# Performance work log

Hardware: AMD Instinct MI355X
Metric: run time of the kernel (lower is better)

## Reference

```python
import jax, jax.numpy as jnp
import numpy as np

HID, QK_NOPE, QK_ROPE, Q_LR, KV_LR, H, V_DIM = 2048, 128, 64, 768, 512, 16, 128
QK_HEAD = QK_NOPE + QK_ROPE
THETA = 10000.0
EPS = 1e-5


def _layernorm(x, g, b):
    mu = jnp.mean(x, axis=-1, keepdims=True)
    var = jnp.mean(jnp.square(x - mu), axis=-1, keepdims=True)
    return (x - mu) * jax.lax.rsqrt(var + EPS) * g + b


def _rotate_half(x):
    x1, x2 = jnp.split(x, 2, axis=-1)
    return jnp.concatenate([-x2, x1], axis=-1)


def setup_inputs() -> dict:
    key = jax.random.key(0)
    ks = jax.random.split(key, 6)
    s = 0.02
    return {
        "hidden_state": jax.random.normal(ks[0], (2, 4096, HID), dtype=jnp.float32),
        "w_qa": jax.random.normal(ks[1], (Q_LR, HID), dtype=jnp.float32) * s,
        "b_qa": jnp.zeros((Q_LR,), jnp.float32),
        "g_qa_ln": jnp.ones((Q_LR,), jnp.float32),
        "b_qa_ln": jnp.zeros((Q_LR,), jnp.float32),
        "w_qb": jax.random.normal(ks[2], (H * QK_HEAD, Q_LR), dtype=jnp.float32) * s,
        "b_qb": jnp.zeros((H * QK_HEAD,), jnp.float32),
        "w_kva": jax.random.normal(ks[3], (KV_LR + QK_ROPE, HID), dtype=jnp.float32) * s,
        "b_kva": jnp.zeros((KV_LR + QK_ROPE,), jnp.float32),
        "g_kva_ln": jnp.ones((KV_LR,), jnp.float32),
        "b_kva_ln": jnp.zeros((KV_LR,), jnp.float32),
        "w_kvb": jax.random.normal(ks[4], (H * (QK_NOPE + V_DIM), KV_LR), dtype=jnp.float32) * s,
        "b_kvb": jnp.zeros((H * (QK_NOPE + V_DIM),), jnp.float32),
    }


def reference(hidden_state, w_qa, b_qa, g_qa_ln, b_qa_ln, w_qb, b_qb,
              w_kva, b_kva, g_kva_ln, b_kva_ln, w_kvb, b_kvb):
    B, S, _ = hidden_state.shape
    # ----- Q path: low-rank down-proj -> LN -> up-proj -----
    q_c = hidden_state @ w_qa.T + b_qa                      # [B,S,Q_LR]
    q_c = _layernorm(q_c, g_qa_ln, b_qa_ln)
    q = (q_c @ w_qb.T + b_qb).reshape(B, S, H, QK_HEAD).transpose(0, 2, 1, 3)  # [B,H,S,QK_HEAD]
    q_nope, q_rope = q[..., :QK_NOPE], q[..., QK_NOPE:]
    # ----- KV path -----
    kv_c = hidden_state @ w_kva.T + b_kva                   # [B,S,KV_LR+ROPE]
    kv_lr, k_rope = kv_c[..., :KV_LR], kv_c[..., KV_LR:]
    kv_lr = _layernorm(kv_lr, g_kva_ln, b_kva_ln)
    kv = (kv_lr @ w_kvb.T + b_kvb).reshape(B, S, H, QK_NOPE + V_DIM).transpose(0, 2, 1, 3)
    k_nope, v = kv[..., :QK_NOPE], kv[..., QK_NOPE:]
    # ----- RoPE on the rope slice only -----
    inv_freq = 1.0 / THETA ** (jnp.arange(0, QK_ROPE, 2, dtype=jnp.float32) / QK_ROPE)
    freq = jnp.arange(S, dtype=jnp.float32)[:, None] * inv_freq[None, :]   # [S, ROPE/2]
    cos = jnp.concatenate([jnp.cos(freq), jnp.cos(freq)], axis=-1)[None, None]  # [1,1,S,ROPE]
    sin = jnp.concatenate([jnp.sin(freq), jnp.sin(freq)], axis=-1)[None, None]
    k_rope = k_rope[:, None]                                # [B,1,S,ROPE]
    q_rot = q_rope * cos + _rotate_half(q_rope) * sin       # [B,H,S,ROPE]
    k_rot = k_rope * cos + _rotate_half(k_rope) * sin       # [B,1,S,ROPE]
    k_rot = jnp.broadcast_to(k_rot, (B, H, S, QK_ROPE))
    q_full = jnp.concatenate([q_nope, q_rot], axis=-1)      # [B,H,S,QK_HEAD]
    k_full = jnp.concatenate([k_nope, k_rot], axis=-1)      # [B,H,S,QK_HEAD]
    # original forward stops after building q,k,v; return them concatenated
    return jnp.concatenate([q_full, k_full, v], axis=-1)    # [B,H,S,2*QK_HEAD+V_DIM]
```

## Files before the change

### kernel.cpp

```cpp
#include <hip/hip_runtime.h>

typedef unsigned short u16;
typedef __bf16 bf16x8 __attribute__((ext_vector_type(8)));
typedef float f32x4 __attribute__((ext_vector_type(4)));


__device__ __forceinline__ u16 f2bf(float f) {
  unsigned u = __float_as_uint(f);
  u += 0x7fffu + ((u >> 16) & 1u);
  return (u16)(u >> 16);
}

__device__ __forceinline__ void load_lds16(const void* g, void* l) {
  __builtin_amdgcn_global_load_lds(
      (const __attribute__((address_space(1))) void*)g,
      (__attribute__((address_space(3))) void*)l, 16, 0, 0);
}

__device__ __forceinline__ void conv_seg(const float* __restrict__ s,
                                         u16* __restrict__ d, int n4,
                                         int g, int stride) {
  const float4* s4 = (const float4*)s;
  ushort4* d4 = (ushort4*)d;
  for (int i = g; i < n4; i += stride) {
    float4 v = s4[i];
    d4[i] = make_ushort4(f2bf(v.x), f2bf(v.y), f2bf(v.z), f2bf(v.w));
  }
}


__global__ __launch_bounds__(256) void prep(
    const float* __restrict__ hid, const float* __restrict__ wqa,
    const float* __restrict__ wkva, const float* __restrict__ wqb,
    const float* __restrict__ wkvb, const float* __restrict__ bqa,
    const float* __restrict__ bkva, u16* __restrict__ hid_b,
    u16* __restrict__ wab_b, u16* __restrict__ wqb_b,
    u16* __restrict__ wkvb_b, float* __restrict__ bias_ab,
    float* __restrict__ cosT, float* __restrict__ sinT) {
  int g = blockIdx.x * 256 + threadIdx.x;
  int stride = gridDim.x * 256;
  conv_seg(hid, hid_b, 4194304, g, stride);
  conv_seg(wqa, wab_b, 393216, g, stride);
  conv_seg(wkva, wab_b + 768 * 2048, 294912, g, stride);
  conv_seg(wqb, wqb_b, 589824, g, stride);
  conv_seg(wkvb, wkvb_b, 524288, g, stride);
  if (g < 1344) bias_ab[g] = (g < 768) ? bqa[g] : bkva[g - 768];
  for (int idx = g; idx < 131072; idx += stride) {
    int s = idx >> 5, i = idx & 31;
    float inv = powf(10000.f, -(float)i / 32.f);
    float f = (float)s * inv;
    float sv, cv;
    sincosf(f, &sv, &cv);
    cosT[idx] = cv;
    sinT[idx] = sv;
  }
}


template <int WHICH>
__global__ __launch_bounds__(256, 2) void gemm_k(
    const u16* __restrict__ A0, const u16* __restrict__ B0,
    const float* __restrict__ bias0, float* __restrict__ C0,
    const u16* __restrict__ qA, const u16* __restrict__ qB,
    const float* __restrict__ qb, const u16* __restrict__ kA,
    const u16* __restrict__ kB, const float* __restrict__ kb,
    float* __restrict__ out, const float* __restrict__ cosT,
    const float* __restrict__ sinT) {
  __shared__ __align__(16) u16 smem[2 * 128 * 64];
  u16* sA = smem;
  u16* sB = smem + 128 * 64;
  const int tid = threadIdx.x;
  const int lane = tid & 63;
  const int wave = tid >> 6;
  const int wm = (wave >> 1) * 64;
  const int wn = (wave & 1) * 64;
  const int lane15 = lane & 15;
  const int quad = lane >> 4;
  const int mTile = blockIdx.x * 128;

  const u16* A;
  const u16* B;
  const float* bias;
  int K, nTile, mode;
  if (WHICH == 0) {
    A = A0; B = B0; bias = bias0; K = 2048; nTile = blockIdx.y * 128; mode = 0;
  } else if (blockIdx.y < 24) {
    A = qA; B = qB; bias = qb; K = 768; nTile = blockIdx.y * 128; mode = 1;
  } else {
    A = kA; B = kB; bias = kb; K = 512; nTile = (blockIdx.y - 24) * 128;
    mode = 2;
  }

  f32x4 acc[4][4] = {};

  const int nStages = K >> 6;
  for (int ks = 0; ks < nStages; ++ks) {
    const int k0 = ks << 6;
    if (ks) __syncthreads();
#pragma unroll
    for (int i = 0; i < 4; ++i) {
      int nu = i * 256 + tid;
      int rr = nu >> 3, u = nu & 7;
      int ul = u ^ (rr & 7);
      load_lds16(A + (size_t)(mTile + rr) * K + (k0 + ul * 8),
                 &sA[(i * 256 + (wave << 6)) * 8]);
    }
#pragma unroll
    for (int i = 0; i < 4; ++i) {
      int nu = i * 256 + tid;
      int rr = nu >> 3, u = nu & 7;
      int ul = u ^ (rr & 7);
      int brow = nTile + rr;
      if (WHICH == 0 && brow >= 1344) brow = 1343;
      load_lds16(B + (size_t)brow * K + (k0 + ul * 8),
                 &sB[(i * 256 + (wave << 6)) * 8]);
    }
    __syncthreads();
#pragma unroll
    for (int kk = 0; kk < 2; ++kk) {
      bf16x8 af[4], bfv[4];
#pragma unroll
      for (int mi = 0; mi < 4; ++mi) {
        int r = wm + mi * 16 + lane15;
        int u = (kk * 4 + quad) ^ (r & 7);
        af[mi] = *(const bf16x8*)&sA[(r * 8 + u) * 8];
      }
#pragma unroll
      for (int ni = 0; ni < 4; ++ni) {
        int r = wn + ni * 16 + lane15;
        int u = (kk * 4 + quad) ^ (r & 7);
        bfv[ni] = *(const bf16x8*)&sB[(r * 8 + u) * 8];
      }
#pragma unroll
      for (int mi = 0; mi < 4; ++mi)
#pragma unroll
        for (int ni = 0; ni < 4; ++ni)
          acc[mi][ni] = __builtin_amdgcn_mfma_f32_16x16x32_bf16(
              af[mi], bfv[ni], acc[mi][ni], 0, 0, 0);
    }
  }

  const int colW = nTile + wn;
  float bv[4];
#pragma unroll
  for (int ni = 0; ni < 4; ++ni) {
    int col = colW + ni * 16 + lane15;
    if (WHICH == 0)
      bv[ni] = (col < 1344) ? bias[col] : 0.f;
    else
      bv[ni] = bias[col];
  }

  int h = 0, ch0 = 0;
  if (mode == 1) {
    h = colW / 192;
    ch0 = colW % 192;
  } else if (mode == 2) {
    int jb = colW & 255;
    h = colW >> 8;
    ch0 = (jb < 128) ? (192 + jb) : (256 + jb);
  }
  const bool ropeTile = (mode == 1) && (ch0 == 128);

  __syncthreads();
  float* lw = (float*)smem + wave * (16 * 68);
  const int hi = lane15 >> 2, l3 = lane15 & 3;

#pragma unroll
  for (int mi = 0; mi < 4; ++mi) {
    f32x4 v[4];
#pragma unroll
    for (int ni = 0; ni < 4; ++ni)
#pragma unroll
      for (int rg = 0; rg < 4; ++rg) v[ni][rg] = acc[mi][ni][rg] + bv[ni];

    if (ropeTile) {
      int rowB = mTile + wm + mi * 16 + quad * 4;
#pragma unroll
      for (int rg = 0; rg < 4; ++rg) {
        int ss = (rowB + rg) & 4095;
#pragma unroll
        for (int ni = 0; ni < 2; ++ni) {
          int i = ni * 16 + lane15;
          float cv = cosT[ss * 32 + i], sv = sinT[ss * 32 + i];
          float x1 = v[ni][rg], x2 = v[ni + 2][rg];
          v[ni][rg] = x1 * cv - x2 * sv;
          v[ni + 2][rg] = x2 * cv + x1 * sv;
        }
      }
    }

    if (mi) asm volatile("s_waitcnt lgkmcnt(0)" ::: "memory");
#pragma unroll
    for (int ni = 0; ni < 4; ++ni) {
      int su = (4 * ni + hi) ^ quad;
#pragma unroll
      for (int rg = 0; rg < 4; ++rg)
        lw[68 * (quad * 4 + rg) + 4 * su + l3] = v[ni][rg];
    }
    asm volatile("s_waitcnt lgkmcnt(0)" ::: "memory");
#pragma unroll
    for (int j = 0; j < 4; ++j) {
      int rr = 4 * j + quad;
      int su = lane15 ^ j;
      float4 o = *(const float4*)&lw[68 * rr + 4 * su];
      int row = mTile + wm + mi * 16 + rr;
      if (mode == 0) {
        if (colW + 4 * lane15 < 1344)
          *(float4*)(C0 + (size_t)row * 1344 + colW + 4 * lane15) = o;
      } else {
        int bb = row >> 12, ss = row & 4095;
        size_t ob =
            ((size_t)((bb * 16 + h) * 4096 + ss)) * 512 + ch0 + 4 * lane15;
        *(float4*)(out + ob) = o;
      }
    }
  }
}


__device__ __forceinline__ void reduce2(float& s1, float& s2, float* rs,
                                        float* rq) {
#pragma unroll
  for (int off = 32; off > 0; off >>= 1) {
    s1 += __shfl_down(s1, off, 64);
    s2 += __shfl_down(s2, off, 64);
  }
  int lane = threadIdx.x & 63, wave = threadIdx.x >> 6;
  if (lane == 0) { rs[wave] = s1; rq[wave] = s2; }
  __syncthreads();
  s1 = rs[0] + rs[1] + rs[2] + rs[3];
  s2 = rq[0] + rq[1] + rq[2] + rq[3];
  __syncthreads();
}

__global__ __launch_bounds__(256) void ln_rot(
    const float* __restrict__ qkvc, const float* __restrict__ g_q,
    const float* __restrict__ b_q, const float* __restrict__ g_kv,
    const float* __restrict__ b_kv, u16* __restrict__ q_ln,
    u16* __restrict__ kv_ln, const float* __restrict__ cosT,
    const float* __restrict__ sinT, float* __restrict__ out) {
  __shared__ float rs[4], rq[4];
  __shared__ __align__(16) float rot[64];
  const int t = blockIdx.x;
  const int tid = threadIdx.x;
  const int bb = t >> 12, ss = t & 4095;
  const float* p = qkvc + (size_t)t * 1344;

  {
    float v[3], sum = 0.f, sq = 0.f;
#pragma unroll
    for (int j = 0; j < 3; ++j) {
      v[j] = p[tid + j * 256];
      sum += v[j];
      sq += v[j] * v[j];
    }
    reduce2(sum, sq, rs, rq);
    float mu = sum * (1.f / 768.f);
    float var = sq * (1.f / 768.f) - mu * mu;
    float inv = rsqrtf(var + 1e-5f);
#pragma unroll
    for (int j = 0; j < 3; ++j) {
      int c = tid + j * 256;
      q_ln[(size_t)t * 768 + c] = f2bf((v[j] - mu) * inv * g_q[c] + b_q[c]);
    }
  }
  {
    float v[2], sum = 0.f, sq = 0.f;
#pragma unroll
    for (int j = 0; j < 2; ++j) {
      v[j] = p[768 + tid + j * 256];
      sum += v[j];
      sq += v[j] * v[j];
    }
    reduce2(sum, sq, rs, rq);
    float mu = sum * (1.f / 512.f);
    float var = sq * (1.f / 512.f) - mu * mu;
    float inv = rsqrtf(var + 1e-5f);
#pragma unroll
    for (int j = 0; j < 2; ++j) {
      int c = tid + j * 256;
      kv_ln[(size_t)t * 512 + c] = f2bf((v[j] - mu) * inv * g_kv[c] + b_kv[c]);
    }
  }
  if (tid < 32) {
    float k1 = p[1280 + tid], k2 = p[1312 + tid];
    float cv = cosT[ss * 32 + tid], sv = sinT[ss * 32 + tid];
    rot[tid] = k1 * cv - k2 * sv;
    rot[tid + 32] = k2 * cv + k1 * sv;
  }
  __syncthreads();
  {
    int hh = tid >> 4, c4 = tid & 15;
    float4 o = ((const float4*)rot)[c4];
    *(float4*)(out + ((size_t)((bb * 16 + hh) * 4096 + ss)) * 512 + 320 +
               4 * c4) = o;
  }
}


extern "C" void kernel_launch(void* const* d_in, const int* in_sizes, int n_in,
                              void* d_out, int out_size, void* d_ws,
                              size_t ws_size, hipStream_t stream) {
  const float* hidden = (const float*)d_in[0];
  const float* w_qa = (const float*)d_in[1];
  const float* b_qa = (const float*)d_in[2];
  const float* g_qa_ln = (const float*)d_in[3];
  const float* b_qa_ln = (const float*)d_in[4];
  const float* w_qb = (const float*)d_in[5];
  const float* b_qb = (const float*)d_in[6];
  const float* w_kva = (const float*)d_in[7];
  const float* b_kva = (const float*)d_in[8];
  const float* g_kva_ln = (const float*)d_in[9];
  const float* b_kva_ln = (const float*)d_in[10];
  const float* w_kvb = (const float*)d_in[11];
  const float* b_kvb = (const float*)d_in[12];
  float* out = (float*)d_out;

  char* ws = (char*)d_ws;
  u16* hid_bf = (u16*)ws;   ws += (size_t)16777216 * 2;
  u16* wab_bf = (u16*)ws;   ws += (size_t)1344 * 2048 * 2;
  u16* wqb_bf = (u16*)ws;   ws += (size_t)2359296 * 2;
  u16* wkvb_bf = (u16*)ws;  ws += (size_t)2097152 * 2;
  float* qkvc = (float*)ws; ws += (size_t)8192 * 1344 * 4;
  u16* q_ln = (u16*)ws;     ws += (size_t)6291456 * 2;
  u16* kv_ln = (u16*)ws;    ws += (size_t)4194304 * 2;
  float* cosT = (float*)ws; ws += (size_t)131072 * 4;
  float* sinT = (float*)ws; ws += (size_t)131072 * 4;
  float* bias_ab = (float*)ws; ws += (size_t)2048 * 4;

  prep<<<dim3(1024), dim3(256), 0, stream>>>(
      hidden, w_qa, w_kva, w_qb, w_kvb, b_qa, b_kva, hid_bf, wab_bf, wqb_bf,
      wkvb_bf, bias_ab, cosT, sinT);
  gemm_k<0><<<dim3(64, 11), dim3(256), 0, stream>>>(
      hid_bf, wab_bf, bias_ab, qkvc, nullptr, nullptr, nullptr, nullptr,
      nullptr, nullptr, nullptr, cosT, sinT);
  ln_rot<<<dim3(8192), dim3(256), 0, stream>>>(qkvc, g_qa_ln, b_qa_ln,
                                               g_kva_ln, b_kva_ln, q_ln, kv_ln,
                                               cosT, sinT, out);
  gemm_k<1><<<dim3(64, 56), dim3(256), 0, stream>>>(
      nullptr, nullptr, nullptr, nullptr, q_ln, wqb_bf, b_qb, kv_ln, wkvb_bf,
      b_kvb, out, cosT, sinT);
}
```

Before: 475.5 us.

## Swizzle GEMM workgroup order, raise occupancy hint, vectorize fused LayerNorm reductions

The GEMM kernel remaps the flat workgroup id so that consecutive blocks are spread in groups of eight across the grid, with the aim of improving L2 reuse of the A/B tiles. The launch-bounds occupancy hint goes from 2 to 3 waves per SIMD, which may force register spills. The LayerNorm/rope kernel now loads float4 vectors and reduces both the Q and KV LayerNorm statistics in a single shuffle pass with one barrier, where it used two passes before. It also writes four packed bf16 values per store. The swizzle assumes gridDim.x is 64 and that the block count is divisible by eight.

```diff
diff --git a/kernel.cpp b/kernel.cpp
--- a/kernel.cpp
+++ b/kernel.cpp
@@ -9,6 +9,10 @@
   unsigned u = __float_as_uint(f);
   u += 0x7fffu + ((u >> 16) & 1u);
   return (u16)(u >> 16);
+}
+
+__device__ __forceinline__ ushort4 f2bf4(float4 v) {
+  return make_ushort4(f2bf(v.x), f2bf(v.y), f2bf(v.z), f2bf(v.w));
 }
 
 __device__ __forceinline__ void load_lds16(const void* g, void* l) {
@@ -58,7 +62,7 @@
 
 
 template <int WHICH>
-__global__ __launch_bounds__(256, 2) void gemm_k(
+__global__ __launch_bounds__(256, 3) void gemm_k(
     const u16* __restrict__ A0, const u16* __restrict__ B0,
     const float* __restrict__ bias0, float* __restrict__ C0,
     const u16* __restrict__ qA, const u16* __restrict__ qB,
@@ -76,18 +80,25 @@
   const int wn = (wave & 1) * 64;
   const int lane15 = lane & 15;
   const int quad = lane >> 4;
-  const int mTile = blockIdx.x * 128;
+
+  const int nwg = gridDim.x * gridDim.y;
+  const int fid = blockIdx.y * 64 + blockIdx.x;
+  const int nfid = (fid & 7) * (nwg >> 3) + (fid >> 3);
+  const int bx = nfid & 63;
+  const int by = nfid >> 6;
+
+  const int mTile = bx * 128;
 
   const u16* A;
   const u16* B;
   const float* bias;
   int K, nTile, mode;
   if (WHICH == 0) {
-    A = A0; B = B0; bias = bias0; K = 2048; nTile = blockIdx.y * 128; mode = 0;
-  } else if (blockIdx.y < 24) {
-    A = qA; B = qB; bias = qb; K = 768; nTile = blockIdx.y * 128; mode = 1;
+    A = A0; B = B0; bias = bias0; K = 2048; nTile = by * 128; mode = 0;
+  } else if (by < 24) {
+    A = qA; B = qB; bias = qb; K = 768; nTile = by * 128; mode = 1;
   } else {
-    A = kA; B = kB; bias = kb; K = 512; nTile = (blockIdx.y - 24) * 128;
+    A = kA; B = kB; bias = kb; K = 512; nTile = (by - 24) * 128;
     mode = 2;
   }
 
@@ -219,71 +230,83 @@
 }
 
 
-__device__ __forceinline__ void reduce2(float& s1, float& s2, float* rs,
-                                        float* rq) {
-#pragma unroll
-  for (int off = 32; off > 0; off >>= 1) {
-    s1 += __shfl_down(s1, off, 64);
-    s2 += __shfl_down(s2, off, 64);
-  }
-  int lane = threadIdx.x & 63, wave = threadIdx.x >> 6;
-  if (lane == 0) { rs[wave] = s1; rq[wave] = s2; }
-  __syncthreads();
-  s1 = rs[0] + rs[1] + rs[2] + rs[3];
-  s2 = rq[0] + rq[1] + rq[2] + rq[3];
-  __syncthreads();
-}
-
 __global__ __launch_bounds__(256) void ln_rot(
     const float* __restrict__ qkvc, const float* __restrict__ g_q,
     const float* __restrict__ b_q, const float* __restrict__ g_kv,
     const float* __restrict__ b_kv, u16* __restrict__ q_ln,
     u16* __restrict__ kv_ln, const float* __restrict__ cosT,
     const float* __restrict__ sinT, float* __restrict__ out) {
-  __shared__ float rs[4], rq[4];
+  __shared__ float red[4][4];
   __shared__ __align__(16) float rot[64];
+  const int tid = threadIdx.x;
   const int t = blockIdx.x;
-  const int tid = threadIdx.x;
   const int bb = t >> 12, ss = t & 4095;
-  const float* p = qkvc + (size_t)t * 1344;
-
-  {
-    float v[3], sum = 0.f, sq = 0.f;
-#pragma unroll
-    for (int j = 0; j < 3; ++j) {
-      v[j] = p[tid + j * 256];
-      sum += v[j];
-      sq += v[j] * v[j];
-    }
-    reduce2(sum, sq, rs, rq);
-    float mu = sum * (1.f / 768.f);
-    float var = sq * (1.f / 768.f) - mu * mu;
-    float inv = rsqrtf(var + 1e-5f);
-#pragma unroll
-    for (int j = 0; j < 3; ++j) {
-      int c = tid + j * 256;
-      q_ln[(size_t)t * 768 + c] = f2bf((v[j] - mu) * inv * g_q[c] + b_q[c]);
-    }
-  }
-  {
-    float v[2], sum = 0.f, sq = 0.f;
-#pragma unroll
-    for (int j = 0; j < 2; ++j) {
-      v[j] = p[768 + tid + j * 256];
-      sum += v[j];
-      sq += v[j] * v[j];
-    }
-    reduce2(sum, sq, rs, rq);
-    float mu = sum * (1.f / 512.f);
-    float var = sq * (1.f / 512.f) - mu * mu;
-    float inv = rsqrtf(var + 1e-5f);
-#pragma unroll
-    for (int j = 0; j < 2; ++j) {
-      int c = tid + j * 256;
-      kv_ln[(size_t)t * 512 + c] = f2bf((v[j] - mu) * inv * g_kv[c] + b_kv[c]);
-    }
+  const float4* p4 = (const float4*)(qkvc + (size_t)t * 1344);
+
+  float4 a = p4[tid];
+  float4 b = make_float4(0.f, 0.f, 0.f, 0.f);
+  if (tid < 80) b = p4[256 + tid];
+
+  float sa = a.x + a.y + a.z + a.w;
+  float sqa = a.x * a.x + a.y * a.y + a.z * a.z + a.w * a.w;
+  float qs = 0.f, qq = 0.f, ks = 0.f, kq = 0.f;
+  if (tid < 192) { qs = sa; qq = sqa; } else { ks = sa; kq = sqa; }
+  if (tid < 64) {
+    ks += b.x + b.y + b.z + b.w;
+    kq += b.x * b.x + b.y * b.y + b.z * b.z + b.w * b.w;
+  }
+#pragma unroll
+  for (int off = 32; off > 0; off >>= 1) {
+    qs += __shfl_down(qs, off, 64);
+    qq += __shfl_down(qq, off, 64);
+    ks += __shfl_down(ks, off, 64);
+    kq += __shfl_down(kq, off, 64);
+  }
+  const int lane = tid & 63, wave = tid >> 6;
+  if (lane == 0) {
+    red[wave][0] = qs; red[wave][1] = qq;
+    red[wave][2] = ks; red[wave][3] = kq;
+  }
+  __syncthreads();
+  qs = red[0][0] + red[1][0] + red[2][0] + red[3][0];
+  qq = red[0][1] + red[1][1] + red[2][1] + red[3][1];
+  ks = red[0][2] + red[1][2] + red[2][2] + red[3][2];
+  kq = red[0][3] + red[1][3] + red[2][3] + red[3][3];
+  const float muq = qs * (1.f / 768.f);
+  const float invq = rsqrtf(qq * (1.f / 768.f) - muq * muq + 1e-5f);
+  const float muk = ks * (1.f / 512.f);
+  const float invk = rsqrtf(kq * (1.f / 512.f) - muk * muk + 1e-5f);
+
+  if (tid < 192) {
+    float4 g = ((const float4*)g_q)[tid];
+    float4 be = ((const float4*)b_q)[tid];
+    float4 o = make_float4((a.x - muq) * invq * g.x + be.x,
+                           (a.y - muq) * invq * g.y + be.y,
+                           (a.z - muq) * invq * g.z + be.z,
+                           (a.w - muq) * invq * g.w + be.w);
+    ((ushort4*)(q_ln + (size_t)t * 768))[tid] = f2bf4(o);
+  } else {
+    int j = tid - 192;
+    float4 g = ((const float4*)g_kv)[j];
+    float4 be = ((const float4*)b_kv)[j];
+    float4 o = make_float4((a.x - muk) * invk * g.x + be.x,
+                           (a.y - muk) * invk * g.y + be.y,
+                           (a.z - muk) * invk * g.z + be.z,
+                           (a.w - muk) * invk * g.w + be.w);
+    ((ushort4*)(kv_ln + (size_t)t * 512))[j] = f2bf4(o);
+  }
+  if (tid < 64) {
+    int j = 64 + tid;
+    float4 g = ((const float4*)g_kv)[j];
+    float4 be = ((const float4*)b_kv)[j];
+    float4 o = make_float4((b.x - muk) * invk * g.x + be.x,
+                           (b.y - muk) * invk * g.y + be.y,
+                           (b.z - muk) * invk * g.z + be.z,
+                           (b.w - muk) * invk * g.w + be.w);
+    ((ushort4*)(kv_ln + (size_t)t * 512))[j] = f2bf4(o);
   }
   if (tid < 32) {
+    const float* p = qkvc + (size_t)t * 1344;
     float k1 = p[1280 + tid], k2 = p[1312 + tid];
     float cv = cosT[ss * 32 + tid], sv = sinT[ss * 32 + tid];
     rot[tid] = k1 * cv - k2 * sv;
```

Result: slower. 535.6 us (+12.6%).
